# Kernel tuning notes

Measured on AMD Instinct MI355X. Metric: run time of the kernel, lower is better.

## Reference

```python
import jax, jax.numpy as jnp
import numpy as np

N, NFEAT, NHID, NHEADS, NCLASS = 8192, 512, 64, 8, 40
ALPHA = 0.2
NEG = jnp.float32(-9e15)


def _gat_layer(h, W, a, concat):
    # h: [N, Fin], W: [Fin, Fout], a: [2*Fout, 1]
    Fout = W.shape[1]
    Wh = h @ W                      # [N, Fout]
    f1 = Wh @ a[:Fout]              # [N, 1]
    f2 = Wh @ a[Fout:]              # [N, 1]
    e = jax.nn.leaky_relu(f1 + f2.T, negative_slope=ALPHA)  # [N, N]
    # NOTE: source masks on e > 0 (adj is NOT used) - replicate faithfully
    att = jax.nn.softmax(jnp.where(e > 0, e, NEG), axis=1)
    h_prime = att @ Wh              # [N, Fout]
    return jax.nn.elu(h_prime) if concat else h_prime


def setup_inputs() -> dict:
    key = jax.random.key(0)
    ks = jax.random.split(key, 6)
    x = jax.random.normal(ks[0], (N, NFEAT), dtype=jnp.float32)
    adj = jax.random.randint(ks[1], (N, N), 0, 2).astype(jnp.bool_)  # unused by math, kept for fidelity
    s = 0.1
    W_heads = jax.random.normal(ks[2], (NHEADS, NFEAT, NHID), dtype=jnp.float32) * s
    a_heads = jax.random.normal(ks[3], (NHEADS, 2 * NHID, 1), dtype=jnp.float32) * s
    W_out = jax.random.normal(ks[4], (NHID * NHEADS, NCLASS), dtype=jnp.float32) * s
    a_out = jax.random.normal(ks[5], (2 * NCLASS, 1), dtype=jnp.float32) * s
    return {"x": x, "adj": adj, "W_heads": W_heads, "a_heads": a_heads,
            "W_out": W_out, "a_out": a_out}


def reference(x, adj, W_heads, a_heads, W_out, a_out):
    # multi-head GAT layers (concat=True), vmapped over heads
    heads = jax.vmap(lambda W, a: _gat_layer(x, W, a, True))(W_heads, a_heads)  # [H, N, NHID]
    h = jnp.transpose(heads, (1, 0, 2)).reshape(N, NHEADS * NHID)
    # output attention layer (concat=False), then elu + log_softmax
    out = _gat_layer(h, W_out, a_out, False)
    out = jax.nn.elu(out)
    return jax.nn.log_softmax(out, axis=1)
```

## Files before the change

kernel.cpp:

```cpp
#include <hip/hip_runtime.h>
#include <math.h>

#define N_NODES 8192
#define NFEAT 512
#define NHID 64
#define NHEADS 8
#define NCLASS 40
#define NCHUNK 128
#define CHUNK 64
#define NB 4096

__global__ __launch_bounds__(256) void gemm1_k(const float* __restrict__ x,
                                               const float* __restrict__ Whw,
                                               const float* __restrict__ a_heads,
                                               float* __restrict__ Wh,
                                               float* __restrict__ f1,
                                               float* __restrict__ f2,
                                               float* __restrict__ meanS) {
  const int head = blockIdx.x;
  const int row0 = blockIdx.y * 64;
  const int tid = threadIdx.x;
  __shared__ float As[32][68];
  __shared__ float Bs[32][64];
  const int tx = tid & 15, ty = tid >> 4;
  float acc[4][4] = {};
  for (int k0 = 0; k0 < NFEAT; k0 += 32) {
    {
      int kk = tid & 31, m0 = (tid >> 5) * 8;
#pragma unroll
      for (int r = 0; r < 8; ++r)
        As[kk][m0 + r] = x[(size_t)(row0 + m0 + r) * NFEAT + k0 + kk];
    }
    {
      int f = tid & 63, c0 = tid >> 6;
#pragma unroll
      for (int r = 0; r < 8; ++r)
        Bs[c0 + r * 4][f] = Whw[(size_t)head * NFEAT * NHID + (size_t)(k0 + c0 + r * 4) * NHID + f];
    }
    __syncthreads();
#pragma unroll
    for (int kk = 0; kk < 32; ++kk) {
      float4 a4 = *reinterpret_cast<const float4*>(&As[kk][ty * 4]);
      float4 b4 = *reinterpret_cast<const float4*>(&Bs[kk][tx * 4]);
      float a[4] = {a4.x, a4.y, a4.z, a4.w};
      float b[4] = {b4.x, b4.y, b4.z, b4.w};
#pragma unroll
      for (int q = 0; q < 4; ++q)
#pragma unroll
        for (int p = 0; p < 4; ++p) acc[q][p] += a[q] * b[p];
    }
    __syncthreads();
  }
#pragma unroll
  for (int q = 0; q < 4; ++q) {
    float4 v = make_float4(acc[q][0], acc[q][1], acc[q][2], acc[q][3]);
    *reinterpret_cast<float4*>(&Wh[(size_t)(row0 + ty * 4 + q) * NFEAT + head * NHID + tx * 4]) = v;
  }
  const float* ah = a_heads + head * 2 * NHID;
  float a1v[4], a2v[4];
#pragma unroll
  for (int p = 0; p < 4; ++p) { a1v[p] = ah[tx * 4 + p]; a2v[p] = ah[NHID + tx * 4 + p]; }
#pragma unroll
  for (int q = 0; q < 4; ++q) {
    float s1 = 0.f, s2 = 0.f;
#pragma unroll
    for (int p = 0; p < 4; ++p) { s1 += acc[q][p] * a1v[p]; s2 += acc[q][p] * a2v[p]; }
#pragma unroll
    for (int m = 1; m < 16; m <<= 1) { s1 += __shfl_xor(s1, m, 64); s2 += __shfl_xor(s2, m, 64); }
    if (tx == 0) {
      int r = row0 + ty * 4 + q;
      f1[(head << 13) + r] = s1;
      f2[(head << 13) + r] = s2;
    }
  }
  __syncthreads();
  float* colp = &As[0][0];
#pragma unroll
  for (int p = 0; p < 4; ++p)
    colp[ty * 64 + tx * 4 + p] = acc[0][p] + acc[1][p] + acc[2][p] + acc[3][p];
  __syncthreads();
  if (tid < 64) {
    float s = 0.f;
#pragma unroll
    for (int yy = 0; yy < 16; ++yy) s += colp[yy * 64 + tid];
    atomicAdd(&meanS[head * NHID + tid], s);
  }
}

__global__ __launch_bounds__(256) void gemm2_k(const float* __restrict__ H,
                                               const float* __restrict__ Wout,
                                               const float* __restrict__ a_out,
                                               float* __restrict__ Wh2,
                                               float* __restrict__ f1b,
                                               float* __restrict__ f2b,
                                               float* __restrict__ meanS2) {
  const int row0 = blockIdx.x * 64;
  const int tid = threadIdx.x;
  __shared__ float As[32][68];
  __shared__ float Bs[32][40];
  __shared__ float cs[NCLASS];
  if (tid < NCLASS) cs[tid] = 0.f;
  const int m = tid >> 2;
  const int n0 = (tid & 3) * 10;
  float acc[10] = {};
  for (int k0 = 0; k0 < NFEAT; k0 += 32) {
    {
      int kk = tid & 31, m0 = (tid >> 5) * 8;
#pragma unroll
      for (int r = 0; r < 8; ++r)
        As[kk][m0 + r] = H[(size_t)(row0 + m0 + r) * NFEAT + k0 + kk];
    }
    {
#pragma unroll
      for (int r = 0; r < 5; ++r) {
        int idx = tid + r * 256;
        int c = idx / 40, n = idx - c * 40;
        Bs[c][n] = Wout[(size_t)(k0 + c) * NCLASS + n];
      }
    }
    __syncthreads();
#pragma unroll
    for (int kk = 0; kk < 32; ++kk) {
      float a = As[kk][m];
#pragma unroll
      for (int q = 0; q < 10; ++q) acc[q] += a * Bs[kk][n0 + q];
    }
    __syncthreads();
  }
#pragma unroll
  for (int q = 0; q < 10; ++q) Wh2[(size_t)(row0 + m) * NCLASS + n0 + q] = acc[q];
  float p1 = 0.f, p2 = 0.f;
#pragma unroll
  for (int q = 0; q < 10; ++q) {
    p1 += acc[q] * a_out[n0 + q];
    p2 += acc[q] * a_out[NCLASS + n0 + q];
  }
  p1 += __shfl_xor(p1, 1, 64); p1 += __shfl_xor(p1, 2, 64);
  p2 += __shfl_xor(p2, 1, 64); p2 += __shfl_xor(p2, 2, 64);
  if ((tid & 3) == 0) { f1b[row0 + m] = p1; f2b[row0 + m] = p2; }
  __syncthreads();
#pragma unroll
  for (int q = 0; q < 10; ++q) atomicAdd(&cs[n0 + q], acc[q]);
  __syncthreads();
  if (tid < NCLASS) atomicAdd(&meanS2[tid], cs[tid]);
}

__global__ __launch_bounds__(1024) void minmax_k(const float* __restrict__ f2, float4* __restrict__ rng) {
  int head = blockIdx.x, tid = threadIdx.x;
  const float* p = f2 + (head << 13);
  float lo = INFINITY, hi = -INFINITY;
  for (int i = tid; i < N_NODES; i += 1024) { float v = p[i]; lo = fminf(lo, v); hi = fmaxf(hi, v); }
  __shared__ float slo[1024], shi[1024];
  slo[tid] = lo; shi[tid] = hi;
  __syncthreads();
  for (int off = 512; off; off >>= 1) {
    if (tid < off) { slo[tid] = fminf(slo[tid], slo[tid + off]); shi[tid] = fmaxf(shi[tid], shi[tid + off]); }
    __syncthreads();
  }
  if (tid == 0) {
    float l = slo[0], h = shi[0];
    float w = fmaxf(h - l, 1e-30f);
    rng[head] = make_float4(l, (float)NB / w, h, 0.f);
  }
}

__global__ __launch_bounds__(256) void hist_k(const float* __restrict__ f2, const float4* __restrict__ rng,
                                              int* __restrict__ hist) {
  int gid = blockIdx.x * 256 + threadIdx.x;
  int head = gid >> 13;
  float v = f2[gid];
  float4 rg = rng[head];
  float u = fminf(fmaxf((v - rg.x) * rg.y, 0.f), (float)(NB - 1));
  atomicAdd(&hist[head * NB + (int)u], 1);
}

__global__ __launch_bounds__(1024) void prefix_k(const int* __restrict__ hist, int* __restrict__ bs) {
  __shared__ int sb[NB];
  int head = blockIdx.x, tid = threadIdx.x;
#pragma unroll
  for (int r = 0; r < NB / 1024; ++r) sb[tid + r * 1024] = hist[head * NB + tid + r * 1024];
  __syncthreads();
  for (int st = 1; st < NB; st <<= 1) {
    int v[NB / 1024];
#pragma unroll
    for (int r = 0; r < NB / 1024; ++r) { int i = tid + r * 1024; v[r] = (i >= st) ? sb[i - st] : 0; }
    __syncthreads();
#pragma unroll
    for (int r = 0; r < NB / 1024; ++r) sb[tid + r * 1024] += v[r];
    __syncthreads();
  }
#pragma unroll
  for (int r = 0; r < NB / 1024; ++r) {
    int b = tid + r * 1024;
    bs[head * (NB + 1) + b] = b ? sb[b - 1] : 0;
  }
  if (tid == 0) bs[head * (NB + 1) + NB] = sb[NB - 1];
}

__global__ __launch_bounds__(256) void scat_k(const float* __restrict__ f2, const float4* __restrict__ rng,
                                              const int* __restrict__ bs, int* __restrict__ cnt,
                                              int* __restrict__ idxs, float* __restrict__ f2s,
                                              float* __restrict__ g) {
  int gid = blockIdx.x * 256 + threadIdx.x;
  int head = gid >> 13, i = gid & 8191;
  float v = f2[gid];
  float4 rg = rng[head];
  float u = fminf(fmaxf((v - rg.x) * rg.y, 0.f), (float)(NB - 1));
  int b = (int)u;
  int pos = bs[head * (NB + 1) + b] + atomicAdd(&cnt[head * NB + b], 1);
  int base = head << 13;
  idxs[base + pos] = i;
  f2s[base + pos] = v;
  g[base + pos] = expf(v - rg.z);
}

template <int F, int LD, int COLSTEP>
__global__ __launch_bounds__(64) void scanA_k(const float* __restrict__ Wh,
                                              const float* __restrict__ g,
                                              const int* __restrict__ idxs,
                                              float* __restrict__ S,
                                              float* __restrict__ D,
                                              float* __restrict__ T,
                                              float* __restrict__ Td) {
  int head = blockIdx.y, chunk = blockIdx.x;
  int lane = threadIdx.x;
  int base = head << 13;
  int kbase = base + chunk * CHUNK;
  int myj = idxs[kbase + lane];
  float myg = g[kbase + lane];
  float acc = 0.f, accD = 0.f;
#pragma unroll
  for (int kk = CHUNK - 1; kk >= 0; --kk) {
    int j = __shfl(myj, kk, 64);
    float gk = __shfl(myg, kk, 64);
    float w = (lane < F) ? Wh[(size_t)j * LD + head * COLSTEP + lane] : 0.f;
    acc += gk * w;
    accD += gk;
    if (lane < F) S[(size_t)(kbase + kk) * F + lane] = acc;
    if (lane == 0) D[kbase + kk] = accD;
  }
  if (lane < F) T[(size_t)(head * NCHUNK + chunk) * F + lane] = acc;
  if (lane == 0) Td[head * NCHUNK + chunk] = accD;
}

template <int F>
__global__ __launch_bounds__(1024) void scanB_k(float* __restrict__ T, float* __restrict__ Td) {
  __shared__ float s[NCHUNK * F];
  __shared__ float td[NCHUNK];
  int head = blockIdx.x;
  int tid = threadIdx.x, slot = tid >> 6, lane = tid & 63;
#pragma unroll
  for (int r = 0; r < 8; ++r) {
    int c = r * 16 + slot;
    if (lane < F) s[c * F + lane] = T[(size_t)(head * NCHUNK + c) * F + lane];
  }
  if (tid < NCHUNK) td[tid] = Td[head * NCHUNK + tid];
  __syncthreads();
  for (int st = 1; st < NCHUNK; st <<= 1) {
    float v[8];
    float tv = 0.f;
#pragma unroll
    for (int r = 0; r < 8; ++r) {
      int c = r * 16 + slot;
      v[r] = (lane < F && c + st < NCHUNK) ? s[(c + st) * F + lane] : 0.f;
    }
    if (tid < NCHUNK && tid + st < NCHUNK) tv = td[tid + st];
    __syncthreads();
#pragma unroll
    for (int r = 0; r < 8; ++r) {
      int c = r * 16 + slot;
      if (lane < F) s[c * F + lane] += v[r];
    }
    if (tid < NCHUNK) td[tid] += tv;
    __syncthreads();
  }
#pragma unroll
  for (int r = 0; r < 8; ++r) {
    int c = r * 16 + slot;
    if (lane < F) T[(size_t)(head * NCHUNK + c) * F + lane] = s[c * F + lane];
  }
  if (tid < NCHUNK) Td[head * NCHUNK + tid] = td[tid];
}

__global__ __launch_bounds__(256) void query1_k(const float* __restrict__ f1,
                                                const float* __restrict__ f2s,
                                                const int* __restrict__ idxs,
                                                const float* __restrict__ Wh,
                                                const float* __restrict__ S,
                                                const float* __restrict__ D,
                                                const float* __restrict__ T,
                                                const float* __restrict__ Td,
                                                const float4* __restrict__ rng,
                                                const int* __restrict__ bs,
                                                const float* __restrict__ meanS,
                                                float* __restrict__ H) {
  int w = blockIdx.x * 4 + (threadIdx.x >> 6);
  int lane = threadIdx.x & 63;
  int head = w & 7, i = w >> 3, base = head << 13;
  float t = f1[base + i];
  float4 rg = rng[head];
  float u = fminf(fmaxf((-t - rg.x) * rg.y, 0.f), (float)(NB - 1));
  int B0 = (int)u;
  int p0 = bs[head * (NB + 1) + B0], p1 = bs[head * (NB + 1) + B0 + 1];
  float num = 0.f, den = 0.f;
  int cnt = N_NODES - p1;
  if (p1 < N_NODES) {
    int c = p1 >> 6;
    num = S[(size_t)(base + p1) * NHID + lane] +
          ((c + 1 < NCHUNK) ? T[(size_t)(head * NCHUNK + c + 1) * NHID + lane] : 0.f);
    den = D[base + p1] + ((c + 1 < NCHUNK) ? Td[head * NCHUNK + c + 1] : 0.f);
  }
  for (int p = p0; p < p1; ++p) {
    float v = f2s[base + p];
    if (t + v > 0.f) {
      int j = idxs[base + p];
      float gk = expf(v - rg.z);
      num += gk * Wh[(size_t)j * NFEAT + head * NHID + lane];
      den += gk;
      ++cnt;
    }
  }
  float val = cnt ? num / den : meanS[head * NHID + lane] * (1.f / N_NODES);
  H[(size_t)i * NFEAT + head * NHID + lane] = (val > 0.f) ? val : expm1f(val);
}

__global__ __launch_bounds__(256) void final_k(const float* __restrict__ f1b,
                                               const float* __restrict__ f2bs,
                                               const int* __restrict__ idx2,
                                               const float* __restrict__ Wh2,
                                               const float* __restrict__ S2,
                                               const float* __restrict__ D2,
                                               const float* __restrict__ T2,
                                               const float* __restrict__ Td2,
                                               const float4* __restrict__ rng2,
                                               const int* __restrict__ bs2,
                                               const float* __restrict__ meanS2,
                                               float* __restrict__ out) {
  int i = blockIdx.x * 4 + (threadIdx.x >> 6);
  int lane = threadIdx.x & 63;
  float t = f1b[i];
  float4 rg = rng2[0];
  float u = fminf(fmaxf((-t - rg.x) * rg.y, 0.f), (float)(NB - 1));
  int B0 = (int)u;
  int p0 = bs2[B0], p1 = bs2[B0 + 1];
  float num = 0.f, den = 0.f;
  int cnt = N_NODES - p1;
  if (p1 < N_NODES) {
    int c = p1 >> 6;
    num = (lane < NCLASS) ? (S2[(size_t)p1 * NCLASS + lane] +
                             ((c + 1 < NCHUNK) ? T2[(size_t)(c + 1) * NCLASS + lane] : 0.f))
                          : 0.f;
    den = D2[p1] + ((c + 1 < NCHUNK) ? Td2[c + 1] : 0.f);
  }
  for (int p = p0; p < p1; ++p) {
    float v = f2bs[p];
    if (t + v > 0.f) {
      int j = idx2[p];
      float gk = expf(v - rg.z);
      if (lane < NCLASS) num += gk * Wh2[(size_t)j * NCLASS + lane];
      den += gk;
      ++cnt;
    }
  }
  float o;
  if (lane < NCLASS) {
    float val = cnt ? num / den : meanS2[lane] * (1.f / N_NODES);
    o = (val > 0.f) ? val : expm1f(val);
  } else {
    o = -INFINITY;
  }
  float m = o;
#pragma unroll
  for (int msk = 32; msk; msk >>= 1) m = fmaxf(m, __shfl_xor(m, msk, 64));
  float e = (lane < NCLASS) ? expf(o - m) : 0.f;
#pragma unroll
  for (int msk = 32; msk; msk >>= 1) e += __shfl_xor(e, msk, 64);
  if (lane < NCLASS) out[(size_t)i * NCLASS + lane] = o - m - logf(e);
}

extern "C" void kernel_launch(void* const* d_in, const int* in_sizes, int n_in,
                              void* d_out, int out_size, void* d_ws, size_t ws_size,
                              hipStream_t stream) {
  const float* x       = (const float*)d_in[0];
  const float* W_heads = (const float*)d_in[2];
  const float* a_heads = (const float*)d_in[3];
  const float* W_out   = (const float*)d_in[4];
  const float* a_out   = (const float*)d_in[5];
  float* out = (float*)d_out;

  float* ws = (float*)d_ws;
  size_t o = 0;
  auto alloc = [&](size_t n) { float* p = ws + o; o += (n + 3) & ~(size_t)3; return p; };
  float*  Wh     = alloc((size_t)N_NODES * NFEAT);
  float*  H      = alloc((size_t)N_NODES * NFEAT);
  float*  S1     = alloc((size_t)NHEADS * N_NODES * NHID);
  float*  f1     = alloc(NHEADS * N_NODES);
  float*  f2     = alloc(NHEADS * N_NODES);
  float*  f2s    = alloc(NHEADS * N_NODES);
  int*    idxs   = (int*)alloc(NHEADS * N_NODES);
  float*  g1     = alloc(NHEADS * N_NODES);
  float*  D1     = alloc(NHEADS * N_NODES);
  float*  T1     = alloc(NHEADS * NCHUNK * NHID);
  float*  Td1    = alloc(NHEADS * NCHUNK);
  float4* rng1   = (float4*)alloc(NHEADS * 4);
  int*    bst1   = (int*)alloc(NHEADS * (NB + 1));
  float*  Wh2    = alloc((size_t)N_NODES * NCLASS);
  float*  S2     = alloc((size_t)N_NODES * NCLASS);
  float*  f1b    = alloc(N_NODES);
  float*  f2b    = alloc(N_NODES);
  float*  f2bs   = alloc(N_NODES);
  int*    idx2   = (int*)alloc(N_NODES);
  float*  g2     = alloc(N_NODES);
  float*  D2     = alloc(N_NODES);
  float*  T2     = alloc(NCHUNK * NCLASS);
  float*  Td2    = alloc(NCHUNK);
  float4* rng2   = (float4*)alloc(4);
  int*    bst2   = (int*)alloc(NB + 1);
  float*  zbase  = ws + o;
  int*    hist1  = (int*)alloc((size_t)NHEADS * NB);
  int*    cnt1   = (int*)alloc((size_t)NHEADS * NB);
  int*    hist2  = (int*)alloc(NB);
  int*    cnt2   = (int*)alloc(NB);
  float*  meanS1 = alloc(NHEADS * NHID);
  float*  meanS2 = alloc(64);
  size_t zbytes = (size_t)((ws + o) - zbase) * sizeof(float);
  hipMemsetAsync(zbase, 0, zbytes, stream);

  gemm1_k<<<dim3(8, 128), 256, 0, stream>>>(x, W_heads, a_heads, Wh, f1, f2, meanS1);
  minmax_k<<<NHEADS, 1024, 0, stream>>>(f2, rng1);
  hist_k<<<(NHEADS * N_NODES) / 256, 256, 0, stream>>>(f2, rng1, hist1);
  prefix_k<<<NHEADS, 1024, 0, stream>>>(hist1, bst1);
  scat_k<<<(NHEADS * N_NODES) / 256, 256, 0, stream>>>(f2, rng1, bst1, cnt1, idxs, f2s, g1);
  scanA_k<NHID, NFEAT, NHID><<<dim3(NCHUNK, NHEADS), 64, 0, stream>>>(Wh, g1, idxs, S1, D1, T1, Td1);
  scanB_k<NHID><<<NHEADS, 1024, 0, stream>>>(T1, Td1);
  query1_k<<<16384, 256, 0, stream>>>(f1, f2s, idxs, Wh, S1, D1, T1, Td1, rng1, bst1, meanS1, H);

  gemm2_k<<<128, 256, 0, stream>>>(H, W_out, a_out, Wh2, f1b, f2b, meanS2);
  minmax_k<<<1, 1024, 0, stream>>>(f2b, rng2);
  hist_k<<<N_NODES / 256, 256, 0, stream>>>(f2b, rng2, hist2);
  prefix_k<<<1, 1024, 0, stream>>>(hist2, bst2);
  scat_k<<<N_NODES / 256, 256, 0, stream>>>(f2b, rng2, bst2, cnt2, idx2, f2bs, g2);
  scanA_k<NCLASS, NCLASS, 0><<<dim3(NCHUNK, 1), 64, 0, stream>>>(Wh2, g2, idx2, S2, D2, T2, Td2);
  scanB_k<NCLASS><<<1, 1024, 0, stream>>>(T2, Td2);
  final_k<<<2048, 256, 0, stream>>>(f1b, f2bs, idx2, Wh2, S2, D2, T2, Td2, rng2, bst2, meanS2, out);
}
```

Baseline: 584.4 us.

## Use split-bf16 MFMA for head GEMM and fuse min/max into GEMM epilogues

The first GEMM now runs on MFMA bf16 instructions. Inputs are split into high and low bf16 parts in a new prep kernel, and three products are accumulated to keep close to fp32 accuracy. The GEMM epilogues compute the per-head f2 min/max through order-preserving encoded atomics, which removes the separate minmax kernels. gemm2 is retiled to 32-row blocks for more blocks. The cost is an extra conversion pass, plus the bf16x3 error in place of exact fp32.

```diff
diff --git a/kernel.cpp b/kernel.cpp
--- a/kernel.cpp
+++ b/kernel.cpp
@@ -10,80 +10,173 @@
 #define CHUNK 64
 #define NB 4096
 
-__global__ __launch_bounds__(256) void gemm1_k(const float* __restrict__ x,
-                                               const float* __restrict__ Whw,
+using bf16x8 = __attribute__((ext_vector_type(8))) short;
+using f32x4 = __attribute__((ext_vector_type(4))) float;
+
+__device__ __forceinline__ ushort f2b(float f) {
+  uint u = __builtin_bit_cast(uint, f);
+  u += 0x7FFFu + ((u >> 16) & 1u);
+  return (ushort)(u >> 16);
+}
+__device__ __forceinline__ float b2f(ushort h) {
+  uint u = (uint)h << 16;
+  return __builtin_bit_cast(float, u);
+}
+__device__ __forceinline__ uint encf(float f) {
+  uint u = __builtin_bit_cast(uint, f);
+  return u ^ ((u >> 31) ? 0xFFFFFFFFu : 0x80000000u);
+}
+__device__ __forceinline__ float decf(uint u) {
+  u ^= ((u >> 31) ? 0x80000000u : 0xFFFFFFFFu);
+  return __builtin_bit_cast(float, u);
+}
+__device__ __forceinline__ float3 load_rng(const uint* mm, int head) {
+  float h = decf(mm[head * 2]);
+  float l = decf(~mm[head * 2 + 1]);
+  float scale = (float)NB / fmaxf(h - l, 1e-30f);
+  return make_float3(l, scale, h);
+}
+__device__ __forceinline__ int bucket_of(float v, float lo, float scale) {
+  float u = fminf(fmaxf((v - lo) * scale, 0.f), (float)(NB - 1));
+  return (int)u;
+}
+
+__global__ __launch_bounds__(256) void prep_k(const float* __restrict__ x,
+                                              const float* __restrict__ W_heads,
+                                              ushort* __restrict__ bth,
+                                              ushort* __restrict__ btl,
+                                              ushort* __restrict__ xh_,
+                                              ushort* __restrict__ xl_) {
+  int b = blockIdx.x, t = threadIdx.x;
+  if (b < 1024) {
+    int gid = b * 256 + t;
+    int n = gid >> 9, c = gid & 511;
+    int h = n >> 6, f = n & 63;
+    float w = W_heads[((size_t)h * NFEAT + c) * NHID + f];
+    ushort hh = f2b(w);
+    bth[gid] = hh;
+    btl[gid] = f2b(w - b2f(hh));
+  } else {
+    int gid2 = (b - 1024) * 256 + t;
+    const float* src = x + (size_t)gid2 * 8;
+    float4 v0 = *reinterpret_cast<const float4*>(src);
+    float4 v1 = *reinterpret_cast<const float4*>(src + 4);
+    float vv[8] = {v0.x, v0.y, v0.z, v0.w, v1.x, v1.y, v1.z, v1.w};
+    uint uh[4], ul[4];
+#pragma unroll
+    for (int k = 0; k < 4; ++k) {
+      ushort h0 = f2b(vv[2 * k]), h1 = f2b(vv[2 * k + 1]);
+      ushort l0 = f2b(vv[2 * k] - b2f(h0)), l1 = f2b(vv[2 * k + 1] - b2f(h1));
+      uh[k] = (uint)h0 | ((uint)h1 << 16);
+      ul[k] = (uint)l0 | ((uint)l1 << 16);
+    }
+    *reinterpret_cast<uint4*>(xh_ + (size_t)gid2 * 8) = make_uint4(uh[0], uh[1], uh[2], uh[3]);
+    *reinterpret_cast<uint4*>(xl_ + (size_t)gid2 * 8) = make_uint4(ul[0], ul[1], ul[2], ul[3]);
+  }
+}
+
+__global__ __launch_bounds__(256) void gemm1_k(const ushort* __restrict__ xh,
+                                               const ushort* __restrict__ xl,
+                                               const ushort* __restrict__ bth,
+                                               const ushort* __restrict__ btl,
                                                const float* __restrict__ a_heads,
                                                float* __restrict__ Wh,
                                                float* __restrict__ f1,
                                                float* __restrict__ f2,
-                                               float* __restrict__ meanS) {
-  const int head = blockIdx.x;
-  const int row0 = blockIdx.y * 64;
+                                               float* __restrict__ meanS,
+                                               uint* __restrict__ mm1) {
+  const int row0 = blockIdx.x * 128, col0 = blockIdx.y * 128;
   const int tid = threadIdx.x;
-  __shared__ float As[32][68];
-  __shared__ float Bs[32][64];
-  const int tx = tid & 15, ty = tid >> 4;
-  float acc[4][4] = {};
+  const int wave = tid >> 6, lane = tid & 63;
+  const int wr = wave >> 1, wc = wave & 1;
+  __shared__ ushort Ah[128 * 40], Al[128 * 40], Bh[128 * 40], Bl[128 * 40];
+  __shared__ float cs[2][64];
+  __shared__ uint lmax[2], lmin[2];
+  if (tid < 2) { lmax[tid] = 0u; lmin[tid] = 0u; }
+  if (tid < 128) cs[tid >> 6][tid & 63] = 0.f;
+  f32x4 acc[4][4] = {};
+  const int sr = tid >> 1, sh = (tid & 1) * 16;
+  const int fr = lane & 15, quad = lane >> 4;
   for (int k0 = 0; k0 < NFEAT; k0 += 32) {
     {
-      int kk = tid & 31, m0 = (tid >> 5) * 8;
-#pragma unroll
-      for (int r = 0; r < 8; ++r)
-        As[kk][m0 + r] = x[(size_t)(row0 + m0 + r) * NFEAT + k0 + kk];
-    }
-    {
-      int f = tid & 63, c0 = tid >> 6;
-#pragma unroll
-      for (int r = 0; r < 8; ++r)
-        Bs[c0 + r * 4][f] = Whw[(size_t)head * NFEAT * NHID + (size_t)(k0 + c0 + r * 4) * NHID + f];
-    }
-    __syncthreads();
-#pragma unroll
-    for (int kk = 0; kk < 32; ++kk) {
-      float4 a4 = *reinterpret_cast<const float4*>(&As[kk][ty * 4]);
-      float4 b4 = *reinterpret_cast<const float4*>(&Bs[kk][tx * 4]);
-      float a[4] = {a4.x, a4.y, a4.z, a4.w};
-      float b[4] = {b4.x, b4.y, b4.z, b4.w};
-#pragma unroll
-      for (int q = 0; q < 4; ++q)
-#pragma unroll
-        for (int p = 0; p < 4; ++p) acc[q][p] += a[q] * b[p];
-    }
-    __syncthreads();
-  }
-#pragma unroll
-  for (int q = 0; q < 4; ++q) {
-    float4 v = make_float4(acc[q][0], acc[q][1], acc[q][2], acc[q][3]);
-    *reinterpret_cast<float4*>(&Wh[(size_t)(row0 + ty * 4 + q) * NFEAT + head * NHID + tx * 4]) = v;
-  }
+      size_t aoff = (size_t)(row0 + sr) * NFEAT + k0 + sh;
+      *reinterpret_cast<uint4*>(&Ah[sr * 40 + sh])     = *reinterpret_cast<const uint4*>(xh + aoff);
+      *reinterpret_cast<uint4*>(&Ah[sr * 40 + sh + 8]) = *reinterpret_cast<const uint4*>(xh + aoff + 8);
+      *reinterpret_cast<uint4*>(&Al[sr * 40 + sh])     = *reinterpret_cast<const uint4*>(xl + aoff);
+      *reinterpret_cast<uint4*>(&Al[sr * 40 + sh + 8]) = *reinterpret_cast<const uint4*>(xl + aoff + 8);
+      size_t boff = (size_t)(col0 + sr) * NFEAT + k0 + sh;
+      *reinterpret_cast<uint4*>(&Bh[sr * 40 + sh])     = *reinterpret_cast<const uint4*>(bth + boff);
+      *reinterpret_cast<uint4*>(&Bh[sr * 40 + sh + 8]) = *reinterpret_cast<const uint4*>(bth + boff + 8);
+      *reinterpret_cast<uint4*>(&Bl[sr * 40 + sh])     = *reinterpret_cast<const uint4*>(btl + boff);
+      *reinterpret_cast<uint4*>(&Bl[sr * 40 + sh + 8]) = *reinterpret_cast<const uint4*>(btl + boff + 8);
+    }
+    __syncthreads();
+    bf16x8 afh[4], afl[4], bfh[4], bfl[4];
+#pragma unroll
+    for (int q = 0; q < 4; ++q) {
+      afh[q] = *reinterpret_cast<const bf16x8*>(&Ah[(wr * 64 + q * 16 + fr) * 40 + quad * 8]);
+      afl[q] = *reinterpret_cast<const bf16x8*>(&Al[(wr * 64 + q * 16 + fr) * 40 + quad * 8]);
+      bfh[q] = *reinterpret_cast<const bf16x8*>(&Bh[(wc * 64 + q * 16 + fr) * 40 + quad * 8]);
+      bfl[q] = *reinterpret_cast<const bf16x8*>(&Bl[(wc * 64 + q * 16 + fr) * 40 + quad * 8]);
+    }
+#pragma unroll
+    for (int qr = 0; qr < 4; ++qr)
+#pragma unroll
+      for (int qc = 0; qc < 4; ++qc) {
+        acc[qr][qc] = __builtin_amdgcn_mfma_f32_16x16x32_bf16(afl[qr], bfh[qc], acc[qr][qc], 0, 0, 0);
+        acc[qr][qc] = __builtin_amdgcn_mfma_f32_16x16x32_bf16(afh[qr], bfl[qc], acc[qr][qc], 0, 0, 0);
+        acc[qr][qc] = __builtin_amdgcn_mfma_f32_16x16x32_bf16(afh[qr], bfh[qc], acc[qr][qc], 0, 0, 0);
+      }
+    __syncthreads();
+  }
+  const int head = blockIdx.y * 2 + wc;
+#pragma unroll
+  for (int qr = 0; qr < 4; ++qr)
+#pragma unroll
+    for (int qc = 0; qc < 4; ++qc)
+#pragma unroll
+      for (int i = 0; i < 4; ++i) {
+        int row = row0 + wr * 64 + qr * 16 + quad * 4 + i;
+        int col = col0 + wc * 64 + qc * 16 + fr;
+        Wh[(size_t)row * NFEAT + col] = acc[qr][qc][i];
+      }
   const float* ah = a_heads + head * 2 * NHID;
   float a1v[4], a2v[4];
 #pragma unroll
-  for (int p = 0; p < 4; ++p) { a1v[p] = ah[tx * 4 + p]; a2v[p] = ah[NHID + tx * 4 + p]; }
-#pragma unroll
-  for (int q = 0; q < 4; ++q) {
-    float s1 = 0.f, s2 = 0.f;
-#pragma unroll
-    for (int p = 0; p < 4; ++p) { s1 += acc[q][p] * a1v[p]; s2 += acc[q][p] * a2v[p]; }
-#pragma unroll
-    for (int m = 1; m < 16; m <<= 1) { s1 += __shfl_xor(s1, m, 64); s2 += __shfl_xor(s2, m, 64); }
-    if (tx == 0) {
-      int r = row0 + ty * 4 + q;
-      f1[(head << 13) + r] = s1;
-      f2[(head << 13) + r] = s2;
-    }
+  for (int qc = 0; qc < 4; ++qc) { a1v[qc] = ah[qc * 16 + fr]; a2v[qc] = ah[NHID + qc * 16 + fr]; }
+#pragma unroll
+  for (int qr = 0; qr < 4; ++qr)
+#pragma unroll
+    for (int i = 0; i < 4; ++i) {
+      float s1 = 0.f, s2 = 0.f;
+#pragma unroll
+      for (int qc = 0; qc < 4; ++qc) { s1 += acc[qr][qc][i] * a1v[qc]; s2 += acc[qr][qc][i] * a2v[qc]; }
+#pragma unroll
+      for (int m = 1; m < 16; m <<= 1) { s1 += __shfl_xor(s1, m, 64); s2 += __shfl_xor(s2, m, 64); }
+      if (fr == 0) {
+        int row = row0 + wr * 64 + qr * 16 + quad * 4 + i;
+        f1[(head << 13) + row] = s1;
+        f2[(head << 13) + row] = s2;
+        atomicMax(&lmax[wc], encf(s2));
+        atomicMax(&lmin[wc], ~encf(s2));
+      }
+    }
+#pragma unroll
+  for (int qc = 0; qc < 4; ++qc) {
+    float v = 0.f;
+#pragma unroll
+    for (int qr = 0; qr < 4; ++qr)
+#pragma unroll
+      for (int i = 0; i < 4; ++i) v += acc[qr][qc][i];
+    v += __shfl_xor(v, 16, 64);
+    v += __shfl_xor(v, 32, 64);
+    if (quad == 0) atomicAdd(&cs[wc][qc * 16 + fr], v);
   }
   __syncthreads();
-  float* colp = &As[0][0];
-#pragma unroll
-  for (int p = 0; p < 4; ++p)
-    colp[ty * 64 + tx * 4 + p] = acc[0][p] + acc[1][p] + acc[2][p] + acc[3][p];
-  __syncthreads();
-  if (tid < 64) {
-    float s = 0.f;
-#pragma unroll
-    for (int yy = 0; yy < 16; ++yy) s += colp[yy * 64 + tid];
-    atomicAdd(&meanS[head * NHID + tid], s);
+  if (tid < 128) atomicAdd(&meanS[(blockIdx.y * 2 + (tid >> 6)) * NHID + (tid & 63)], cs[tid >> 6][tid & 63]);
+  if (tid < 2) {
+    atomicMax(&mm1[(blockIdx.y * 2 + tid) * 2], lmax[tid]);
+    atomicMax(&mm1[(blockIdx.y * 2 + tid) * 2 + 1], lmin[tid]);
   }
 }
 
@@ -93,29 +186,34 @@
                                                float* __restrict__ Wh2,
                                                float* __restrict__ f1b,
                                                float* __restrict__ f2b,
-                                               float* __restrict__ meanS2) {
-  const int row0 = blockIdx.x * 64;
+                                               float* __restrict__ meanS2,
+                                               uint* __restrict__ mm2) {
+  const int row0 = blockIdx.x * 32;
   const int tid = threadIdx.x;
-  __shared__ float As[32][68];
+  __shared__ float As[32][33];
   __shared__ float Bs[32][40];
   __shared__ float cs[NCLASS];
+  __shared__ uint lmax, lmin;
   if (tid < NCLASS) cs[tid] = 0.f;
-  const int m = tid >> 2;
-  const int n0 = (tid & 3) * 10;
-  float acc[10] = {};
+  if (tid == 0) { lmax = 0u; lmin = 0u; }
+  const int m = tid >> 3;
+  const int n0 = (tid & 7) * 5;
+  float acc[5] = {};
   for (int k0 = 0; k0 < NFEAT; k0 += 32) {
     {
-      int kk = tid & 31, m0 = (tid >> 5) * 8;
-#pragma unroll
-      for (int r = 0; r < 8; ++r)
-        As[kk][m0 + r] = H[(size_t)(row0 + m0 + r) * NFEAT + k0 + kk];
+      int kk = tid & 31, mq = tid >> 5;
+#pragma unroll
+      for (int r = 0; r < 4; ++r)
+        As[kk][mq * 4 + r] = H[(size_t)(row0 + mq * 4 + r) * NFEAT + k0 + kk];
     }
     {
 #pragma unroll
       for (int r = 0; r < 5; ++r) {
         int idx = tid + r * 256;
-        int c = idx / 40, n = idx - c * 40;
-        Bs[c][n] = Wout[(size_t)(k0 + c) * NCLASS + n];
+        if (idx < 1280) {
+          int c = idx / 40, n = idx - c * 40;
+          Bs[c][n] = Wout[(size_t)(k0 + c) * NCLASS + n];
+        }
       }
     }
     __syncthreads();
@@ -123,55 +221,39 @@
     for (int kk = 0; kk < 32; ++kk) {
       float a = As[kk][m];
 #pragma unroll
-      for (int q = 0; q < 10; ++q) acc[q] += a * Bs[kk][n0 + q];
-    }
-    __syncthreads();
-  }
-#pragma unroll
-  for (int q = 0; q < 10; ++q) Wh2[(size_t)(row0 + m) * NCLASS + n0 + q] = acc[q];
+      for (int q = 0; q < 5; ++q) acc[q] += a * Bs[kk][n0 + q];
+    }
+    __syncthreads();
+  }
+#pragma unroll
+  for (int q = 0; q < 5; ++q) Wh2[(size_t)(row0 + m) * NCLASS + n0 + q] = acc[q];
   float p1 = 0.f, p2 = 0.f;
 #pragma unroll
-  for (int q = 0; q < 10; ++q) {
+  for (int q = 0; q < 5; ++q) {
     p1 += acc[q] * a_out[n0 + q];
     p2 += acc[q] * a_out[NCLASS + n0 + q];
   }
-  p1 += __shfl_xor(p1, 1, 64); p1 += __shfl_xor(p1, 2, 64);
-  p2 += __shfl_xor(p2, 1, 64); p2 += __shfl_xor(p2, 2, 64);
-  if ((tid & 3) == 0) { f1b[row0 + m] = p1; f2b[row0 + m] = p2; }
-  __syncthreads();
-#pragma unroll
-  for (int q = 0; q < 10; ++q) atomicAdd(&cs[n0 + q], acc[q]);
+  p1 += __shfl_xor(p1, 1, 64); p1 += __shfl_xor(p1, 2, 64); p1 += __shfl_xor(p1, 4, 64);
+  p2 += __shfl_xor(p2, 1, 64); p2 += __shfl_xor(p2, 2, 64); p2 += __shfl_xor(p2, 4, 64);
+  if ((tid & 7) == 0) {
+    f1b[row0 + m] = p1;
+    f2b[row0 + m] = p2;
+    atomicMax(&lmax, encf(p2));
+    atomicMax(&lmin, ~encf(p2));
+  }
+#pragma unroll
+  for (int q = 0; q < 5; ++q) atomicAdd(&cs[n0 + q], acc[q]);
   __syncthreads();
   if (tid < NCLASS) atomicAdd(&meanS2[tid], cs[tid]);
-}
-
-__global__ __launch_bounds__(1024) void minmax_k(const float* __restrict__ f2, float4* __restrict__ rng) {
-  int head = blockIdx.x, tid = threadIdx.x;
-  const float* p = f2 + (head << 13);
-  float lo = INFINITY, hi = -INFINITY;
-  for (int i = tid; i < N_NODES; i += 1024) { float v = p[i]; lo = fminf(lo, v); hi = fmaxf(hi, v); }
-  __shared__ float slo[1024], shi[1024];
-  slo[tid] = lo; shi[tid] = hi;
-  __syncthreads();
-  for (int off = 512; off; off >>= 1) {
-    if (tid < off) { slo[tid] = fminf(slo[tid], slo[tid + off]); shi[tid] = fmaxf(shi[tid], shi[tid + off]); }
-    __syncthreads();
-  }
-  if (tid == 0) {
-    float l = slo[0], h = shi[0];
-    float w = fmaxf(h - l, 1e-30f);
-    rng[head] = make_float4(l, (float)NB / w, h, 0.f);
-  }
-}
-
-__global__ __launch_bounds__(256) void hist_k(const float* __restrict__ f2, const float4* __restrict__ rng,
+  if (tid == 0) { atomicMax(&mm2[0], lmax); atomicMax(&mm2[1], lmin); }
+}
+
+__global__ __launch_bounds__(256) void hist_k(const float* __restrict__ f2, const uint* __restrict__ mm,
                                               int* __restrict__ hist) {
   int gid = blockIdx.x * 256 + threadIdx.x;
   int head = gid >> 13;
-  float v = f2[gid];
-  float4 rg = rng[head];
-  float u = fminf(fmaxf((v - rg.x) * rg.y, 0.f), (float)(NB - 1));
-  atomicAdd(&hist[head * NB + (int)u], 1);
+  float3 rg = load_rng(mm, head);
+  atomicAdd(&hist[head * NB + bucket_of(f2[gid], rg.x, rg.y)], 1);
 }
 
 __global__ __launch_bounds__(1024) void prefix_k(const int* __restrict__ hist, int* __restrict__ bs) {
@@ -197,16 +279,15 @@
   if (tid == 0) bs[head * (NB + 1) + NB] = sb[NB - 1];
 }
 
-__global__ __launch_bounds__(256) void scat_k(const float* __restrict__ f2, const float4* __restrict__ rng,
+__global__ __launch_bounds__(256) void scat_k(const float* __restrict__ f2, const uint* __restrict__ mm,
                                               const int* __restrict__ bs, int* __restrict__ cnt,
                                               int* __restrict__ idxs, float* __restrict__ f2s,
                                               float* __restrict__ g) {
   int gid = blockIdx.x * 256 + threadIdx.x;
   int head = gid >> 13, i = gid & 8191;
   float v = f2[gid];
-  float4 rg = rng[head];
-  float u = fminf(fmaxf((v - rg.x) * rg.y, 0.f), (float)(NB - 1));
-  int b = (int)u;
+  float3 rg = load_rng(mm, head);
+  int b = bucket_of(v, rg.x, rg.y);
   int pos = bs[head * (NB + 1) + b] + atomicAdd(&cnt[head * NB + b], 1);
   int base = head << 13;
   idxs[base + pos] = i;
@@ -220,7 +301,7 @@
                                               const int* __restrict__ idxs,
                                               float* __restrict__ S,
                                               float* __restrict__ D,
-                                              float* __restrict__ T,
+                                              float* __restrict__ T_,
                                               float* __restrict__ Td) {
   int head = blockIdx.y, chunk = blockIdx.x;
   int lane = threadIdx.x;
@@ -239,12 +320,12 @@
     if (lane < F) S[(size_t)(kbase + kk) * F + lane] = acc;
     if (lane == 0) D[kbase + kk] = accD;
   }
-  if (lane < F) T[(size_t)(head * NCHUNK + chunk) * F + lane] = acc;
+  if (lane < F) T_[(size_t)(head * NCHUNK + chunk) * F + lane] = acc;
   if (lane == 0) Td[head * NCHUNK + chunk] = accD;
 }
 
 template <int F>
-__global__ __launch_bounds__(1024) void scanB_k(float* __restrict__ T, float* __restrict__ Td) {
+__global__ __launch_bounds__(1024) void scanB_k(float* __restrict__ T_, float* __restrict__ Td) {
   __shared__ float s[NCHUNK * F];
   __shared__ float td[NCHUNK];
   int head = blockIdx.x;
@@ -252,7 +333,7 @@
 #pragma unroll
   for (int r = 0; r < 8; ++r) {
     int c = r * 16 + slot;
-    if (lane < F) s[c * F + lane] = T[(size_t)(head * NCHUNK + c) * F + lane];
+    if (lane < F) s[c * F + lane] = T_[(size_t)(head * NCHUNK + c) * F + lane];
   }
   if (tid < NCHUNK) td[tid] = Td[head * NCHUNK + tid];
   __syncthreads();
@@ -277,7 +358,7 @@
 #pragma unroll
   for (int r = 0; r < 8; ++r) {
     int c = r * 16 + slot;
-    if (lane < F) T[(size_t)(head * NCHUNK + c) * F + lane] = s[c * F + lane];
+    if (lane < F) T_[(size_t)(head * NCHUNK + c) * F + lane] = s[c * F + lane];
   }
   if (tid < NCHUNK) Td[head * NCHUNK + tid] = td[tid];
 }
@@ -288,9 +369,9 @@
                                                 const float* __restrict__ Wh,
                                                 const float* __restrict__ S,
                                                 const float* __restrict__ D,
-                                                const float* __restrict__ T,
+                                                const float* __restrict__ T_,
                                                 const float* __restrict__ Td,
-                                                const float4* __restrict__ rng,
+                                                const uint* __restrict__ mm,
                                                 const int* __restrict__ bs,
                                                 const float* __restrict__ meanS,
                                                 float* __restrict__ H) {
@@ -298,16 +379,15 @@
   int lane = threadIdx.x & 63;
   int head = w & 7, i = w >> 3, base = head << 13;
   float t = f1[base + i];
-  float4 rg = rng[head];
-  float u = fminf(fmaxf((-t - rg.x) * rg.y, 0.f), (float)(NB - 1));
-  int B0 = (int)u;
+  float3 rg = load_rng(mm, head);
+  int B0 = bucket_of(-t, rg.x, rg.y);
   int p0 = bs[head * (NB + 1) + B0], p1 = bs[head * (NB + 1) + B0 + 1];
   float num = 0.f, den = 0.f;
   int cnt = N_NODES - p1;
   if (p1 < N_NODES) {
     int c = p1 >> 6;
     num = S[(size_t)(base + p1) * NHID + lane] +
-          ((c + 1 < NCHUNK) ? T[(size_t)(head * NCHUNK + c + 1) * NHID + lane] : 0.f);
+          ((c + 1 < NCHUNK) ? T_[(size_t)(head * NCHUNK + c + 1) * NHID + lane] : 0.f);
     den = D[base + p1] + ((c + 1 < NCHUNK) ? Td[head * NCHUNK + c + 1] : 0.f);
   }
   for (int p = p0; p < p1; ++p) {
@@ -332,16 +412,15 @@
                                                const float* __restrict__ D2,
                                                const float* __restrict__ T2,
                                                const float* __restrict__ Td2,
-                                               const float4* __restrict__ rng2,
+                                               const uint* __restrict__ mm2,
                                                const int* __restrict__ bs2,
                                                const float* __restrict__ meanS2,
                                                float* __restrict__ out) {
   int i = blockIdx.x * 4 + (threadIdx.x >> 6);
   int lane = threadIdx.x & 63;
   float t = f1b[i];
-  float4 rg = rng2[0];
-  float u = fminf(fmaxf((-t - rg.x) * rg.y, 0.f), (float)(NB - 1));
-  int B0 = (int)u;
+  float3 rg = load_rng(mm2, 0);
+  int B0 = bucket_of(-t, rg.x, rg.y);
   int p0 = bs2[B0], p1 = bs2[B0 + 1];
   float num = 0.f, den = 0.f;
   int cnt = N_NODES - p1;
@@ -391,9 +470,13 @@
   float* ws = (float*)d_ws;
   size_t o = 0;
   auto alloc = [&](size_t n) { float* p = ws + o; o += (n + 3) & ~(size_t)3; return p; };
+  float*  S1     = alloc((size_t)NHEADS * N_NODES * NHID);
+  ushort* xh     = (ushort*)S1;
+  ushort* xl     = (ushort*)(S1 + (size_t)N_NODES * NFEAT / 2);
+  ushort* BTh    = (ushort*)alloc((size_t)NFEAT * NFEAT / 2);
+  ushort* BTl    = (ushort*)alloc((size_t)NFEAT * NFEAT / 2);
   float*  Wh     = alloc((size_t)N_NODES * NFEAT);
   float*  H      = alloc((size_t)N_NODES * NFEAT);
-  float*  S1     = alloc((size_t)NHEADS * N_NODES * NHID);
   float*  f1     = alloc(NHEADS * N_NODES);
   float*  f2     = alloc(NHEADS * N_NODES);
   float*  f2s    = alloc(NHEADS * N_NODES);
@@ -402,7 +485,6 @@
   float*  D1     = alloc(NHEADS * N_NODES);
   float*  T1     = alloc(NHEADS * NCHUNK * NHID);
   float*  Td1    = alloc(NHEADS * NCHUNK);
-  float4* rng1   = (float4*)alloc(NHEADS * 4);
   int*    bst1   = (int*)alloc(NHEADS * (NB + 1));
   float*  Wh2    = alloc((size_t)N_NODES * NCLASS);
   float*  S2     = alloc((size_t)N_NODES * NCLASS);
@@ -414,33 +496,33 @@
   float*  D2     = alloc(N_NODES);
   float*  T2     = alloc(NCHUNK * NCLASS);
   float*  Td2    = alloc(NCHUNK);
-  float4* rng2   = (float4*)alloc(4);
   int*    bst2   = (int*)alloc(NB + 1);
   float*  zbase  = ws + o;
   int*    hist1  = (int*)alloc((size_t)NHEADS * NB);
   int*    cnt1   = (int*)alloc((size_t)NHEADS * NB);
   int*    hist2  = (int*)alloc(NB);
   int*    cnt2   = (int*)alloc(NB);
+  uint*   mm1    = (uint*)alloc(16);
+  uint*   mm2    = (uint*)alloc(4);
   float*  meanS1 = alloc(NHEADS * NHID);
   float*  meanS2 = alloc(64);
   size_t zbytes = (size_t)((ws + o) - zbase) * sizeof(float);
   hipMemsetAsync(zbase, 0, zbytes, stream);
 
-  gemm1_k<<<dim3(8, 128), 256, 0, stream>>>(x, W_heads, a_heads, Wh, f1, f2, meanS1);
-  minmax_k<<<NHEADS, 1024, 0, stream>>>(f2, rng1);
-  hist_k<<<(NHEADS * N_NODES) / 256, 256, 0, stream>>>(f2, rng1, hist1);
+  prep_k<<<1024 + 2048, 256, 0, stream>>>(x, W_heads, BTh, BTl, xh, xl);
+  gemm1_k<<<dim3(64, 4), 256, 0, stream>>>(xh, xl, BTh, BTl, a_heads, Wh, f1, f2, meanS1, mm1);
+  hist_k<<<(NHEADS * N_NODES) / 256, 256, 0, stream>>>(f2, mm1, hist1);
   prefix_k<<<NHEADS, 1024, 0, stream>>>(hist1, bst1);
-  scat_k<<<(NHEADS * N_NODES) / 256, 256, 0, stream>>>(f2, rng1, bst1, cnt1, idxs, f2s, g1);
+  scat_k<<<(NHEADS * N_NODES) / 256, 256, 0, stream>>>(f2, mm1, bst1, cnt1, idxs, f2s, g1);
   scanA_k<NHID, NFEAT, NHID><<<dim3(NCHUNK, NHEADS), 64, 0, stream>>>(Wh, g1, idxs, S1, D1, T1, Td1);
   scanB_k<NHID><<<NHEADS, 1024, 0, stream>>>(T1, Td1);
-  query1_k<<<16384, 256, 0, stream>>>(f1, f2s, idxs, Wh, S1, D1, T1, Td1, rng1, bst1, meanS1, H);
-
-  gemm2_k<<<128, 256, 0, stream>>>(H, W_out, a_out, Wh2, f1b, f2b, meanS2);
-  minmax_k<<<1, 1024, 0, stream>>>(f2b, rng2);
-  hist_k<<<N_NODES / 256, 256, 0, stream>>>(f2b, rng2, hist2);
+  query1_k<<<16384, 256, 0, stream>>>(f1, f2s, idxs, Wh, S1, D1, T1, Td1, mm1, bst1, meanS1, H);
+
+  gemm2_k<<<256, 256, 0, stream>>>(H, W_out, a_out, Wh2, f1b, f2b, meanS2, mm2);
+  hist_k<<<N_NODES / 256, 256, 0, stream>>>(f2b, mm2, hist2);
   prefix_k<<<1, 1024, 0, stream>>>(hist2, bst2);
-  scat_k<<<N_NODES / 256, 256, 0, stream>>>(f2b, rng2, bst2, cnt2, idx2, f2bs, g2);
+  scat_k<<<N_NODES / 256, 256, 0, stream>>>(f2b, mm2, bst2, cnt2, idx2, f2bs, g2);
   scanA_k<NCLASS, NCLASS, 0><<<dim3(NCHUNK, 1), 64, 0, stream>>>(Wh2, g2, idx2, S2, D2, T2, Td2);
   scanB_k<NCLASS><<<1, 1024, 0, stream>>>(T2, Td2);
-  final_k<<<2048, 256, 0, stream>>>(f1b, f2bs, idx2, Wh2, S2, D2, T2, Td2, rng2, bst2, meanS2, out);
-}
+  final_k<<<2048, 256, 0, stream>>>(f1b, f2bs, idx2, Wh2, S2, D2, T2, Td2, mm2, bst2, meanS2, out);
+}
```

Measured after the change: 561.1 us. -4.0%, faster.
